# Kernel tuning notes

Measured on AMD Instinct MI355X. Metric: run time of the kernel, lower is better.

Reference implementation:

```python
import jax, jax.numpy as jnp
import numpy as np

B, IMGS, PH, PW = 4, 4, 16, 16      # 4 groups, 4 images/group, 16x16 patches per image
P, C = 16, 3
N = IMGS * PH * PW                   # 1024 packed tokens per group
PATCH_DIM = C * P * P                # 768
DIM, HEADS, DHEAD, DEPTH = 768, 12, 64, 4
INNER = HEADS * DHEAD
MLP = 3072
POSMAX = 32                          # image_size // patch_size
NCLS = 1000
SCALE = DHEAD ** 0.5


def _ln(x, g):
    # torch LayerNorm with learned gamma, beta frozen at 0
    mu = jnp.mean(x, -1, keepdims=True)
    var = jnp.var(x, -1, keepdims=True)
    return (x - mu) * jax.lax.rsqrt(var + 1e-5) * g


def _qk_rmsnorm(t, g):
    # F.normalize(t, dim=-1) * sqrt(dhead) * gamma[h, 1, d]; t: (b,h,n,d), g: (h,d)
    nrm = jnp.sqrt(jnp.sum(t * t, -1, keepdims=True))
    return t / jnp.maximum(nrm, 1e-12) * SCALE * g[None, :, None, :]


def _attention(x, context, ln_g, Wq, Wkv, qg, kg, Wo, attn_mask):
    xn = _ln(x, ln_g)
    kv_in = xn if context is None else context  # context is NOT normed (matches torch)
    q = xn @ Wq
    k, v = jnp.split(kv_in @ Wkv, 2, axis=-1)
    split = lambda t: t.reshape(t.shape[0], t.shape[1], HEADS, DHEAD).transpose(0, 2, 1, 3)
    q, k, v = split(q), split(k), split(v)
    q = _qk_rmsnorm(q, qg)
    k = _qk_rmsnorm(k, kg)
    dots = jnp.einsum('bhid,bhjd->bhij', q, k)  # no 1/sqrt(d): scale lives in RMSNorm
    dots = jnp.where(attn_mask, dots, -jnp.finfo(dots.dtype).max)
    attn = jax.nn.softmax(dots, axis=-1)
    out = jnp.einsum('bhij,bhjd->bhid', attn, v)
    out = out.transpose(0, 2, 1, 3).reshape(x.shape[0], -1, INNER)
    return out @ Wo


def _forward(patches, emb_ln_g, W_emb, b_emb, emb_ln2_g, pos_h, pos_w,
             ln_attn_g, Wq, Wkv, qn_g, kn_g, Wo,
             ln_ff_g, W1, b1, W2, b2, final_ln_g,
             pool_q, pool_ln_g, pWq, pWkv, p_qn_g, p_kn_g, pWo,
             head_ln_g, W_head,
             patch_positions, image_ids, lengths):
    valid = jnp.arange(N)[None, :] < lengths[:, None]              # (B,N) True = real token
    same_img = image_ids[:, :, None] == image_ids[:, None, :]      # (B,i,j) block-diagonal
    attn_mask = (same_img & valid[:, None, :])[:, None]            # (B,1,i,j)

    x = _ln(patches, emb_ln_g) @ W_emb + b_emb
    x = _ln(x, emb_ln2_g)
    x = x + pos_h[patch_positions[..., 0]] + pos_w[patch_positions[..., 1]]

    for l in range(DEPTH):
        x = _attention(x, None, ln_attn_g[l], Wq[l], Wkv[l], qn_g[l], kn_g[l], Wo[l], attn_mask) + x
        h = jax.nn.gelu(_ln(x, ln_ff_g[l]) @ W1[l] + b1[l], approximate=False)
        x = h @ W2[l] + b2[l] + x
    x = _ln(x, final_ln_g)

    # attention pooling: one learned query per packed image
    queries = jnp.broadcast_to(pool_q, (x.shape[0], IMGS, DIM))
    pool_mask = ((jnp.arange(IMGS)[None, :, None] == image_ids[:, None, :]) & valid[:, None, :])[:, None]
    pooled = _attention(queries, x, pool_ln_g, pWq, pWkv, p_qn_g, p_kn_g, pWo, pool_mask) + queries
    return _ln(pooled, head_ln_g) @ W_head  # (B, IMGS, NCLS), mlp_head has no bias


def setup_inputs():
    key = jax.random.key(0)
    ks = jax.random.split(key, 20)
    rn = lambda k, shape, s=0.02: (jax.random.normal(k, shape) * s).astype(jnp.float32)

    patches = jax.random.normal(ks[0], (B, N, PATCH_DIM), dtype=jnp.float32)
    hh, ww = jnp.meshgrid(jnp.arange(PH), jnp.arange(PW), indexing='ij')
    pos = jnp.stack([hh.reshape(-1), ww.reshape(-1)], axis=-1)        # (256,2)
    patch_positions = jnp.broadcast_to(jnp.tile(pos, (IMGS, 1))[None], (B, N, 2)).astype(jnp.int32)
    image_ids = jnp.broadcast_to(jnp.repeat(jnp.arange(IMGS), PH * PW)[None], (B, N)).astype(jnp.int32)
    lengths = jnp.full((B,), N, dtype=jnp.int32)

    return dict(
        patches=patches, patch_positions=patch_positions, image_ids=image_ids, lengths=lengths,
        emb_ln_g=jnp.ones(PATCH_DIM, jnp.float32), W_emb=rn(ks[1], (PATCH_DIM, DIM)),
        b_emb=jnp.zeros(DIM, jnp.float32), emb_ln2_g=jnp.ones(DIM, jnp.float32),
        pos_h=rn(ks[2], (POSMAX, DIM), 1.0), pos_w=rn(ks[3], (POSMAX, DIM), 1.0),
        ln_attn_g=jnp.ones((DEPTH, DIM), jnp.float32),
        Wq=rn(ks[4], (DEPTH, DIM, INNER)), Wkv=rn(ks[5], (DEPTH, DIM, 2 * INNER)),
        qn_g=jnp.ones((DEPTH, HEADS, DHEAD), jnp.float32), kn_g=jnp.ones((DEPTH, HEADS, DHEAD), jnp.float32),
        Wo=rn(ks[6], (DEPTH, INNER, DIM)),
        ln_ff_g=jnp.ones((DEPTH, DIM), jnp.float32),
        W1=rn(ks[7], (DEPTH, DIM, MLP)), b1=jnp.zeros((DEPTH, MLP), jnp.float32),
        W2=rn(ks[8], (DEPTH, MLP, DIM)), b2=jnp.zeros((DEPTH, DIM), jnp.float32),
        final_ln_g=jnp.ones(DIM, jnp.float32),
        pool_q=rn(ks[9], (DIM,), 1.0), pool_ln_g=jnp.ones(DIM, jnp.float32),
        pWq=rn(ks[10], (DIM, INNER)), pWkv=rn(ks[11], (DIM, 2 * INNER)),
        p_qn_g=jnp.ones((HEADS, DHEAD), jnp.float32), p_kn_g=jnp.ones((HEADS, DHEAD), jnp.float32),
        pWo=rn(ks[12], (INNER, DIM)),
        head_ln_g=jnp.ones(DIM, jnp.float32), W_head=rn(ks[13], (DIM, NCLS)),
    )


def reference(patches, patch_positions, image_ids, lengths,
              emb_ln_g, W_emb, b_emb, emb_ln2_g, pos_h, pos_w,
              ln_attn_g, Wq, Wkv, qn_g, kn_g, Wo,
              ln_ff_g, W1, b1, W2, b2, final_ln_g,
              pool_q, pool_ln_g, pWq, pWkv, p_qn_g, p_kn_g, pWo,
              head_ln_g, W_head):
    return _forward(patches, emb_ln_g, W_emb, b_emb, emb_ln2_g, pos_h, pos_w,
                    ln_attn_g, Wq, Wkv, qn_g, kn_g, Wo,
                    ln_ff_g, W1, b1, W2, b2, final_ln_g,
                    pool_q, pool_ln_g, pWq, pWkv, p_qn_g, p_kn_g, pWo,
                    head_ln_g, W_head, patch_positions, image_ids, lengths)
```

## Files before the change

### kernel.cpp

```cpp
#include <hip/hip_runtime.h>
#include <hip/hip_bf16.h>
#include <math.h>

using bf16 = __hip_bfloat16;
typedef short s16x8 __attribute__((ext_vector_type(8)));
typedef float f32x4 __attribute__((ext_vector_type(4)));

#define DEVI __device__ __forceinline__

static constexpr int NB    = 4;
static constexpr int NTOK  = 1024;
static constexpr int DIM   = 768;
static constexpr int NH    = 12;
static constexpr int MLPD  = 3072;
static constexpr int NLAYER= 4;
static constexpr int NIMG  = 4;
static constexpr int NCLS  = 1000;
static constexpr int MR    = NB * NTOK;

DEVI float b2f(bf16 v){ return __bfloat162float(v); }
DEVI bf16  f2b(float v){ return __float2bfloat16(v); }

DEVI void async16(const void* g, void* l) {
  __builtin_amdgcn_global_load_lds((const __attribute__((address_space(1))) void*)g,
                                   (__attribute__((address_space(3))) void*)l, 16, 0, 0);
}

DEVI f32x4 mfma16(s16x8 a, s16x8 b, f32x4 c) {
  return __builtin_amdgcn_mfma_f32_16x16x32_bf16(a, b, c, 0, 0, 0);
}

DEVI float block_sum(float v, float* scratch, int tid) {
  #pragma unroll
  for (int o = 32; o >= 1; o >>= 1) v += __shfl_xor(v, o);
  __syncthreads();
  if ((tid & 63) == 0) scratch[tid >> 6] = v;
  __syncthreads();
  return scratch[0] + scratch[1] + scratch[2] + scratch[3];
}

DEVI float block_max(float v, float* scratch, int tid) {
  #pragma unroll
  for (int o = 32; o >= 1; o >>= 1) v = fmaxf(v, __shfl_xor(v, o));
  __syncthreads();
  if ((tid & 63) == 0) scratch[tid >> 6] = v;
  __syncthreads();
  return fmaxf(fmaxf(scratch[0], scratch[1]), fmaxf(scratch[2], scratch[3]));
}

struct bh4 { bf16 a, b, c, d; };
struct TEntry { const float* src; bf16* dst; int R, C, tiles, tC; };
struct TDesc  { TEntry e[22]; };

__global__ __launch_bounds__(256) void transpose_kernel(TDesc D, int nent) {
  int bid = blockIdx.x, ei = 0;
  while (ei < nent - 1 && bid >= D.e[ei].tiles) { bid -= D.e[ei].tiles; ++ei; }
  const TEntry E = D.e[ei];
  const int tr = bid / E.tC, tc = bid % E.tC;
  __shared__ bf16 t[32][33];
  const int tid = threadIdx.x;
  const int lr = tid >> 3, lc = (tid & 7) * 4;
  const float* srow = E.src + (size_t)(tr*32 + lr)*E.C + tc*32 + lc;
  float4 v = *(const float4*)srow;
  t[lr][lc] = f2b(v.x); t[lr][lc+1] = f2b(v.y); t[lr][lc+2] = f2b(v.z); t[lr][lc+3] = f2b(v.w);
  __syncthreads();
  bh4 o;
  o.a = t[lc+0][lr]; o.b = t[lc+1][lr]; o.c = t[lc+2][lr]; o.d = t[lc+3][lr];
  *(bh4*)(E.dst + (size_t)(tc*32 + lr)*E.R + tr*32 + lc) = o;
}

__global__ __launch_bounds__(256) void ln768_kernel(const float* __restrict__ in,
    const float* __restrict__ g, bf16* __restrict__ out)
{
  __shared__ float scratch[4];
  const int row = blockIdx.x, tid = threadIdx.x;
  const float* p = in + (size_t)row*768;
  const float v0 = p[tid], v1 = p[tid+256], v2 = p[tid+512];
  const float s  = block_sum(v0+v1+v2, scratch, tid);
  const float ss = block_sum(v0*v0+v1*v1+v2*v2, scratch, tid);
  const float mu = s * (1.0f/768.0f);
  const float var = ss * (1.0f/768.0f) - mu*mu;
  const float rstd = rsqrtf(var + 1e-5f);
  bf16* o = out + (size_t)row*768;
  o[tid]     = f2b((v0-mu)*rstd*g[tid]);
  o[tid+256] = f2b((v1-mu)*rstd*g[tid+256]);
  o[tid+512] = f2b((v2-mu)*rstd*g[tid+512]);
}

__global__ __launch_bounds__(256) void ln_pos_kernel(const float* __restrict__ in,
    const float* __restrict__ g, const float* __restrict__ pos_h, const float* __restrict__ pos_w,
    const int* __restrict__ ppos, float* __restrict__ out)
{
  __shared__ float scratch[4];
  const int row = blockIdx.x, tid = threadIdx.x;
  const float* p = in + (size_t)row*768;
  const float v0 = p[tid], v1 = p[tid+256], v2 = p[tid+512];
  const float s  = block_sum(v0+v1+v2, scratch, tid);
  const float ss = block_sum(v0*v0+v1*v1+v2*v2, scratch, tid);
  const float mu = s * (1.0f/768.0f);
  const float rstd = rsqrtf(ss*(1.0f/768.0f) - mu*mu + 1e-5f);
  const int p0 = ppos[row*2], p1 = ppos[row*2+1];
  const float* ph = pos_h + (size_t)p0*768;
  const float* pw = pos_w + (size_t)p1*768;
  float* o = out + (size_t)row*768;
  o[tid]     = (v0-mu)*rstd*g[tid]     + ph[tid]     + pw[tid];
  o[tid+256] = (v1-mu)*rstd*g[tid+256] + ph[tid+256] + pw[tid+256];
  o[tid+512] = (v2-mu)*rstd*g[tid+512] + ph[tid+512] + pw[tid+512];
}

template<int DO_BIAS, int DO_GELU, int OUT_BF16, int DO_RES, int NTILE>
__global__ __launch_bounds__(256)
void gemm_mfma(const bf16* __restrict__ A, const bf16* __restrict__ BT,
               const float* __restrict__ bias, float* __restrict__ Cf,
               bf16* __restrict__ Cb, int M, int Nn, int K)
{
  constexpr int NF = NTILE / 32;
  __shared__ bf16 As[2][64*64];
  __shared__ bf16 Bs[2][(NTILE/2)*64];
  const int tid = threadIdx.x;
  const int wid = tid >> 6, lane = tid & 63;
  const int quad = lane >> 4, l15 = lane & 15;
  const int wy = wid >> 1, wx = wid & 1;
  const int m0 = blockIdx.y * 128, n0 = blockIdx.x * NTILE;
  const int rl = lane >> 3;
  const int cs = lane & 7;

  f32x4 acc[4][NF];
  #pragma unroll
  for (int i = 0; i < 4; ++i)
    #pragma unroll
    for (int j = 0; j < NF; ++j) acc[i][j] = (f32x4){0.f,0.f,0.f,0.f};

  auto stage = [&](int buf, int k0) {
    #pragma unroll
    for (int c = 0; c < 2; ++c) {
      const int rbase = wid*8 + c*32;
      const int r_abs = rbase + rl;
      const int ceff  = cs ^ (r_abs & 7);
      const int mg    = 2*r_abs + (ceff >> 2);
      const int jb    = (ceff & 3) * 16;
      async16((const char*)A + ((size_t)(m0 + mg)*K + k0)*2 + jb, (char*)As[buf] + rbase*128);
    }
    #pragma unroll
    for (int c = 0; c < NTILE/64; ++c) {
      const int rbase = wid*8 + c*32;
      const int r_abs = rbase + rl;
      const int ceff  = cs ^ (r_abs & 7);
      const int ng    = 2*r_abs + (ceff >> 2);
      const int jb    = (ceff & 3) * 16;
      async16((const char*)BT + ((size_t)(n0 + ng)*K + k0)*2 + jb, (char*)Bs[buf] + rbase*128);
    }
  };

  const int nk = K >> 5;
  stage(0, 0);
  for (int kt = 0; kt < nk; ++kt) {
    const int cb = kt & 1;
    __syncthreads();
    if (kt + 1 < nk) stage(cb ^ 1, (kt + 1) << 5);
    s16x8 af[4], bfr[NF];
    #pragma unroll
    for (int mt = 0; mt < 4; ++mt) {
      const int m = wy*64 + mt*16 + l15;
      const int r = m >> 1;
      const int cq = (((m & 1) << 2) | quad) ^ (r & 7);
      af[mt] = *(const s16x8*)((const char*)As[cb] + r*128 + cq*16);
    }
    #pragma unroll
    for (int nt = 0; nt < NF; ++nt) {
      const int n = wx*(NTILE/2) + nt*16 + l15;
      const int r = n >> 1;
      const int cq = (((n & 1) << 2) | quad) ^ (r & 7);
      bfr[nt] = *(const s16x8*)((const char*)Bs[cb] + r*128 + cq*16);
    }
    #pragma unroll
    for (int mt = 0; mt < 4; ++mt)
      #pragma unroll
      for (int nt = 0; nt < NF; ++nt)
        acc[mt][nt] = mfma16(af[mt], bfr[nt], acc[mt][nt]);
  }

  #pragma unroll
  for (int nt = 0; nt < NF; ++nt) {
    const int col = n0 + wx*(NTILE/2) + nt*16 + l15;
    float bv = 0.f;
    if constexpr (DO_BIAS) bv = bias[col];
    #pragma unroll
    for (int mt = 0; mt < 4; ++mt) {
      #pragma unroll
      for (int r = 0; r < 4; ++r) {
        const int row = m0 + wy*64 + mt*16 + quad*4 + r;
        float v = acc[mt][nt][r];
        if constexpr (DO_BIAS) v += bv;
        if constexpr (DO_GELU) v = 0.5f*v*(1.0f + erff(v*0.70710678118654752f));
        const size_t idx = (size_t)row*Nn + col;
        if constexpr (OUT_BF16) Cb[idx] = f2b(v);
        else if constexpr (DO_RES) Cf[idx] += v;
        else Cf[idx] = v;
      }
    }
  }
}

template<int IN_BF16, int DO_BIAS>
__global__ __launch_bounds__(256) void smallm_gemm(const void* __restrict__ Xv,
    const float* __restrict__ W, const float* __restrict__ bias,
    float* __restrict__ out, int Nn)
{
  __shared__ float Xs[16*768];
  __shared__ float red[4][16][64];
  const int tid = threadIdx.x;
  if constexpr (IN_BF16) {
    const bf16* X = (const bf16*)Xv;
    for (int i = tid; i < 16*768; i += 256) Xs[i] = b2f(X[i]);
  } else {
    const float* X = (const float*)Xv;
    for (int i = tid; i < 16*768; i += 256) Xs[i] = X[i];
  }
  __syncthreads();
  const int cl = tid & 63, kg = tid >> 6;
  const int c = blockIdx.x*64 + cl;
  float acc[16];
  #pragma unroll
  for (int r = 0; r < 16; ++r) acc[r] = 0.f;
  if (c < Nn) {
    const int k0 = kg*192;
    #pragma unroll 4
    for (int k = k0; k < k0 + 192; ++k) {
      const float w = W[(size_t)k*Nn + c];
      #pragma unroll
      for (int r = 0; r < 16; ++r) acc[r] += Xs[r*768 + k] * w;
    }
  }
  #pragma unroll
  for (int r = 0; r < 16; ++r) red[kg][r][cl] = acc[r];
  __syncthreads();
  if (kg == 0 && c < Nn) {
    #pragma unroll
    for (int r = 0; r < 16; ++r) {
      float v = red[0][r][cl] + red[1][r][cl] + red[2][r][cl] + red[3][r][cl];
      if constexpr (DO_BIAS) v += bias[c];
      out[(size_t)r*Nn + c] = v;
    }
  }
}

__global__ __launch_bounds__(256) void rms_qkv_kernel(const float* __restrict__ qkv,
    const float* __restrict__ qg, const float* __restrict__ kg,
    bf16* __restrict__ Qb, bf16* __restrict__ Kb, bf16* __restrict__ VTb)
{
  __shared__ float tile[64*68];
  const int nt = blockIdx.x, h = blockIdx.y, b = blockIdx.z;
  const int tid = threadIdx.x;
  const int bh = b*NH + h;
  const size_t rowbase = (size_t)(b*NTOK + nt*64);
  const int r = tid >> 2, pp = tid & 3;

  auto stage = [&](int off) {
    #pragma unroll
    for (int rr = 0; rr < 4; ++rr) {
      const int idx = rr*256 + tid;
      const int rw = idx >> 4, c4 = (idx & 15) << 2;
      float4 val = *(const float4*)(qkv + (rowbase + rw)*2304 + off + c4);
      *(float4*)(&tile[rw*68 + c4]) = val;
    }
  };

  stage(h*64);
  __syncthreads();
  {
    float ssq = 0.f;
    #pragma unroll
    for (int i = 0; i < 16; ++i) { float x = tile[r*68 + pp*16 + i]; ssq += x*x; }
    ssq += __shfl_xor(ssq, 1); ssq += __shfl_xor(ssq, 2);
    const float rn = 8.0f / fmaxf(sqrtf(ssq), 1e-12f);
    bf16* orow = Qb + ((size_t)bh*NTOK + nt*64 + r)*64;
    #pragma unroll
    for (int i = 0; i < 16; ++i) { int d = pp*16+i; orow[d] = f2b(tile[r*68+d]*rn*qg[h*64+d]); }
  }
  __syncthreads();
  stage(768 + h*64);
  __syncthreads();
  {
    float ssq = 0.f;
    #pragma unroll
    for (int i = 0; i < 16; ++i) { float x = tile[r*68 + pp*16 + i]; ssq += x*x; }
    ssq += __shfl_xor(ssq, 1); ssq += __shfl_xor(ssq, 2);
    const float rn = 8.0f / fmaxf(sqrtf(ssq), 1e-12f);
    bf16* orow = Kb + ((size_t)bh*NTOK + nt*64 + r)*64;
    #pragma unroll
    for (int i = 0; i < 16; ++i) { int d = pp*16+i; orow[d] = f2b(tile[r*68+d]*rn*kg[h*64+d]); }
  }
  __syncthreads();
  stage(1536 + h*64);
  __syncthreads();
  {
    const int d = tid >> 2;
    bf16* orow = VTb + ((size_t)bh*64 + d)*NTOK + nt*64;
    #pragma unroll
    for (int i = 0; i < 16; ++i) { int n = pp*16 + i; orow[n] = f2b(tile[n*68 + d]); }
  }
}

__global__ __launch_bounds__(256) void attn_mfma(const bf16* __restrict__ Qb,
    const bf16* __restrict__ Kb, const bf16* __restrict__ VTb, bf16* __restrict__ Ob,
    const int* __restrict__ ids, const int* __restrict__ lens)
{
  __shared__ bf16 Ps[4][16*72];
  __shared__ int  ids_s[NTOK];
  const int qt = blockIdx.x, h = blockIdx.y, b = blockIdx.z;
  const int tid = threadIdx.x;
  const int wid = tid >> 6, lane = tid & 63;
  const int quad = lane >> 4, l15 = lane & 15;
  const int bh = b*NH + h;
  const int q0 = qt*64;
  const int len = lens[b];

  #pragma unroll
  for (int i = 0; i < 4; ++i) ids_s[i*256 + tid] = ids[b*NTOK + i*256 + tid];
  __syncthreads();

  const bf16* qrow = Qb + ((size_t)bh*NTOK + q0 + wid*16 + l15)*64;
  const s16x8 aq0 = *(const s16x8*)(qrow + quad*8);
  const s16x8 aq1 = *(const s16x8*)(qrow + 32 + quad*8);

  int idq[4];
  #pragma unroll
  for (int rr = 0; rr < 4; ++rr) idq[rr] = ids_s[q0 + wid*16 + quad*4 + rr];

  unsigned qm = 0;
  #pragma unroll
  for (int rr = 0; rr < 4; ++rr) qm |= 1u << (idq[rr] & 31);
  #pragma unroll
  for (int o = 32; o >= 1; o >>= 1) qm |= (unsigned)__shfl_xor((int)qm, o);

  f32x4 oacc[4];
  #pragma unroll
  for (int nt = 0; nt < 4; ++nt) oacc[nt] = (f32x4){0.f,0.f,0.f,0.f};
  float mrow[4] = {-3.0e38f,-3.0e38f,-3.0e38f,-3.0e38f};
  float lrow[4] = {0.f,0.f,0.f,0.f};

  const bf16* Kgb = Kb  + (size_t)bh*NTOK*64;
  const bf16* Vgb = VTb + (size_t)bh*64*NTOK;
  bf16* pw = Ps[wid];

  for (int kt = 0; kt < 16; ++kt) {
    const int k0 = kt*64;
    const int idk_l = ids_s[k0 + lane];
    const bool ok = ((k0 + lane) < len) && (((qm >> (idk_l & 31)) & 1u) != 0u);
    if (__ballot(ok) == 0ULL) continue;

    f32x4 sA[4];
    #pragma unroll
    for (int jt = 0; jt < 4; ++jt) {
      const bf16* krow = Kgb + (size_t)(k0 + jt*16 + l15)*64;
      const s16x8 bk0 = *(const s16x8*)(krow + quad*8);
      const s16x8 bk1 = *(const s16x8*)(krow + 32 + quad*8);
      f32x4 s = (f32x4){0.f,0.f,0.f,0.f};
      s = mfma16(aq0, bk0, s);
      s = mfma16(aq1, bk1, s);
      sA[jt] = s;
    }
    #pragma unroll
    for (int jt = 0; jt < 4; ++jt) {
      const int j = k0 + jt*16 + l15;
      const int idk = ids_s[j];
      const bool kvld = j < len;
      #pragma unroll
      for (int rr = 0; rr < 4; ++rr)
        sA[jt][rr] = (kvld && idk == idq[rr]) ? sA[jt][rr] : -3.0e38f;
    }
    float alpha[4], mnew[4];
    #pragma unroll
    for (int rr = 0; rr < 4; ++rr) {
      float mx = fmaxf(fmaxf(sA[0][rr], sA[1][rr]), fmaxf(sA[2][rr], sA[3][rr]));
      mx = fmaxf(mx, __shfl_xor(mx, 1));
      mx = fmaxf(mx, __shfl_xor(mx, 2));
      mx = fmaxf(mx, __shfl_xor(mx, 4));
      mx = fmaxf(mx, __shfl_xor(mx, 8));
      const float mn = fmaxf(mrow[rr], mx);
      mnew[rr] = mn;
      alpha[rr] = expf(mrow[rr] - mn);
      mrow[rr] = mn;
    }
    #pragma unroll
    for (int rr = 0; rr < 4; ++rr) {
      float rs = 0.f;
      #pragma unroll
      for (int jt = 0; jt < 4; ++jt) {
        const float pv = (sA[jt][rr] > -1.0e38f) ? expf(sA[jt][rr] - mnew[rr]) : 0.0f;
        sA[jt][rr] = pv;
        rs += pv;
      }
      rs += __shfl_xor(rs, 1);
      rs += __shfl_xor(rs, 2);
      rs += __shfl_xor(rs, 4);
      rs += __shfl_xor(rs, 8);
      lrow[rr] = lrow[rr]*alpha[rr] + rs;
      #pragma unroll
      for (int nt = 0; nt < 4; ++nt) oacc[nt][rr] *= alpha[rr];
    }
    #pragma unroll
    for (int jt = 0; jt < 4; ++jt)
      #pragma unroll
      for (int rr = 0; rr < 4; ++rr)
        pw[(quad*4+rr)*72 + jt*16 + l15] = f2b(sA[jt][rr]);
    #pragma unroll
    for (int ss = 0; ss < 2; ++ss) {
      const s16x8 ap = *(const s16x8*)(pw + l15*72 + ss*32 + quad*8);
      #pragma unroll
      for (int nt = 0; nt < 4; ++nt) {
        const s16x8 bv = *(const s16x8*)(Vgb + (size_t)(nt*16 + l15)*NTOK + k0 + ss*32 + quad*8);
        oacc[nt] = mfma16(ap, bv, oacc[nt]);
      }
    }
  }

  #pragma unroll
  for (int rr = 0; rr < 4; ++rr) {
    const float inv = lrow[rr] > 0.f ? 1.0f/lrow[rr] : 0.0f;
    const int n = q0 + wid*16 + quad*4 + rr;
    bf16* orow = Ob + ((size_t)b*NTOK + n)*768 + h*64;
    #pragma unroll
    for (int nt = 0; nt < 4; ++nt)
      orow[nt*16 + l15] = f2b(oacc[nt][rr]*inv);
  }
}

__global__ __launch_bounds__(256) void pool_q_kernel(const float* __restrict__ pool_q,
    const float* __restrict__ pool_ln_g, const float* __restrict__ pWq,
    const float* __restrict__ p_qn_g, float* __restrict__ qp)
{
  __shared__ float xn[768];
  __shared__ float scratch[4];
  __shared__ float qraw[64];
  const int h = blockIdx.x, tid = threadIdx.x;
  float v0 = pool_q[tid], v1 = pool_q[tid+256], v2 = pool_q[tid+512];
  const float s  = block_sum(v0+v1+v2, scratch, tid);
  const float ss = block_sum(v0*v0+v1*v1+v2*v2, scratch, tid);
  const float mu = s*(1.0f/768.0f);
  const float rstd = rsqrtf(ss*(1.0f/768.0f) - mu*mu + 1e-5f);
  xn[tid]     = (v0-mu)*rstd*pool_ln_g[tid];
  xn[tid+256] = (v1-mu)*rstd*pool_ln_g[tid+256];
  xn[tid+512] = (v2-mu)*rstd*pool_ln_g[tid+512];
  __syncthreads();
  const int d = tid >> 2, pp = tid & 3;
  const int col = h*64 + d;
  float acc = 0.f;
  for (int k = pp*192; k < (pp+1)*192; ++k) acc += xn[k]*pWq[(size_t)k*768 + col];
  acc += __shfl_xor(acc, 1); acc += __shfl_xor(acc, 2);
  if (pp == 0) qraw[d] = acc;
  __syncthreads();
  if (tid < 64) {
    const float q = qraw[tid];
    float sq = q*q;
    #pragma unroll
    for (int o = 32; o >= 1; o >>= 1) sq += __shfl_xor(sq, o);
    const float rn = 8.0f / fmaxf(sqrtf(sq), 1e-12f);
    qp[h*64 + tid] = q * rn * p_qn_g[h*64 + tid];
  }
}

__global__ __launch_bounds__(256) void pool_attn_kernel(const float* __restrict__ kvp,
    const float* __restrict__ qp, const float* __restrict__ kg,
    const int* __restrict__ ids, const int* __restrict__ lens, float* __restrict__ pooled)
{
  __shared__ float sp[1024];
  __shared__ float qg_s[64];
  __shared__ float scratch[4];
  __shared__ float outred[4][64];
  const int h = blockIdx.x, img = blockIdx.y, b = blockIdx.z;
  const int tid = threadIdx.x;
  const int len = lens[b];
  if (tid < 64) qg_s[tid] = qp[h*64 + tid] * kg[h*64 + tid];
  __syncthreads();

  float smax = -3.0e38f;
  for (int j = tid; j < 1024; j += 256) {
    float sv = -3.0e38f;
    if (j < len && ids[b*NTOK + j] == img) {
      const float* kr = kvp + (size_t)(b*NTOK + j)*1536 + h*64;
      float ssq = 0.f, dq = 0.f;
      #pragma unroll
      for (int dd = 0; dd < 64; dd += 4) {
        float4 k4 = *(const float4*)(kr + dd);
        ssq += k4.x*k4.x + k4.y*k4.y + k4.z*k4.z + k4.w*k4.w;
        dq  += qg_s[dd]*k4.x + qg_s[dd+1]*k4.y + qg_s[dd+2]*k4.z + qg_s[dd+3]*k4.w;
      }
      const float rn = 8.0f / fmaxf(sqrtf(ssq), 1e-12f);
      sv = dq * rn;
    }
    sp[j] = sv;
    smax = fmaxf(smax, sv);
  }
  const float M = block_max(smax, scratch, tid);
  float lsum = 0.f;
  for (int j = tid; j < 1024; j += 256) {
    const float p = (sp[j] > -1.0e38f) ? expf(sp[j] - M) : 0.0f;
    sp[j] = p;
    lsum += p;
  }
  const float L = block_sum(lsum, scratch, tid);
  const float invL = L > 0.f ? 1.0f / L : 0.0f;

  const int d = tid & 63, jg = tid >> 6;
  float acc = 0.f;
  for (int j = jg; j < 1024; j += 4) {
    const float p = sp[j];
    if (p > 0.f) acc += p * kvp[(size_t)(b*NTOK + j)*1536 + 768 + h*64 + d];
  }
  outred[jg][d] = acc;
  __syncthreads();
  if (tid < 64) {
    const float o = (outred[0][tid] + outred[1][tid] + outred[2][tid] + outred[3][tid]) * invL;
    pooled[((size_t)b*NIMG + img)*768 + h*64 + tid] = o;
  }
}

extern "C" void kernel_launch(void* const* d_in, const int* in_sizes, int n_in,
                              void* d_out, int out_size, void* d_ws, size_t ws_size,
                              hipStream_t stream)
{
  const float* patches    = (const float*)d_in[0];
  const int*   ppos       = (const int*)d_in[1];
  const int*   image_ids  = (const int*)d_in[2];
  const int*   lengths    = (const int*)d_in[3];
  const float* emb_ln_g   = (const float*)d_in[4];
  const float* W_emb      = (const float*)d_in[5];
  const float* b_emb      = (const float*)d_in[6];
  const float* emb_ln2_g  = (const float*)d_in[7];
  const float* pos_h      = (const float*)d_in[8];
  const float* pos_w      = (const float*)d_in[9];
  const float* ln_attn_g  = (const float*)d_in[10];
  const float* Wq         = (const float*)d_in[11];
  const float* Wkv        = (const float*)d_in[12];
  const float* qn_g       = (const float*)d_in[13];
  const float* kn_g       = (const float*)d_in[14];
  const float* Wo         = (const float*)d_in[15];
  const float* ln_ff_g    = (const float*)d_in[16];
  const float* W1         = (const float*)d_in[17];
  const float* b1         = (const float*)d_in[18];
  const float* W2         = (const float*)d_in[19];
  const float* b2v        = (const float*)d_in[20];
  const float* final_ln_g = (const float*)d_in[21];
  const float* pool_q     = (const float*)d_in[22];
  const float* pool_ln_g  = (const float*)d_in[23];
  const float* pWq        = (const float*)d_in[24];
  const float* pWkv       = (const float*)d_in[25];
  const float* p_qn_g     = (const float*)d_in[26];
  const float* p_kn_g     = (const float*)d_in[27];
  const float* pWo        = (const float*)d_in[28];
  const float* head_ln_g  = (const float*)d_in[29];
  const float* W_head     = (const float*)d_in[30];

  char* ws = (char*)d_ws;
  size_t off = 0;
  auto alloc = [&](size_t sz){ size_t r = off; off += (sz + 255) & ~(size_t)255; return r; };

  const size_t o_WembT = alloc((size_t)768*768*2);
  size_t o_QKVT[4], o_WoT[4], o_W1T[4], o_W2T[4];
  for (int l = 0; l < NLAYER; ++l) {
    o_QKVT[l] = alloc((size_t)2304*768*2);
    o_WoT[l]  = alloc((size_t)768*768*2);
    o_W1T[l]  = alloc((size_t)3072*768*2);
    o_W2T[l]  = alloc((size_t)768*3072*2);
  }
  const size_t o_pWkvT = alloc((size_t)1536*768*2);
  const size_t o_x     = alloc((size_t)MR*768*4);
  const size_t o_xn    = alloc((size_t)MR*768*2);
  const size_t o_qkv   = alloc((size_t)MR*2304*4);
  const size_t o_Qb    = alloc((size_t)MR*768*2);
  const size_t o_Kb    = alloc((size_t)MR*768*2);
  const size_t o_VT    = alloc((size_t)MR*768*2);
  const size_t o_Ob    = alloc((size_t)MR*768*2);
  const size_t o_qp    = alloc((size_t)768*4);
  const size_t o_pool  = alloc((size_t)16*768*4);
  const size_t o_poolf = alloc((size_t)16*768*4);
  const size_t o_hl    = alloc((size_t)16*768*2);
  if (off > ws_size) return;

  float* x    = (float*)(ws + o_x);
  bf16*  xn   = (bf16*)(ws + o_xn);
  float* qkv  = (float*)(ws + o_qkv);
  bf16*  hb   = (bf16*)(ws + o_qkv);
  bf16*  Qb   = (bf16*)(ws + o_Qb);
  bf16*  Kb   = (bf16*)(ws + o_Kb);
  bf16*  VTb  = (bf16*)(ws + o_VT);
  bf16*  Ob   = (bf16*)(ws + o_Ob);
  float* qp   = (float*)(ws + o_qp);
  float* pooled  = (float*)(ws + o_pool);
  float* pooledf = (float*)(ws + o_poolf);
  bf16*  hl   = (bf16*)(ws + o_hl);

  TDesc td; int ne = 0, total = 0;
  auto add = [&](const float* s, size_t dofs, int R, int C){
    td.e[ne].src = s;
    td.e[ne].dst = (bf16*)(ws + dofs);
    td.e[ne].R = R; td.e[ne].C = C;
    td.e[ne].tiles = (R/32)*(C/32); td.e[ne].tC = C/32;
    total += td.e[ne].tiles; ++ne;
  };
  add(W_emb, o_WembT, 768, 768);
  for (int l = 0; l < NLAYER; ++l) {
    add(Wq  + (size_t)l*768*768,  o_QKVT[l],                 768, 768);
    add(Wkv + (size_t)l*768*1536, o_QKVT[l] + (size_t)768*768*2, 768, 1536);
    add(Wo  + (size_t)l*768*768,  o_WoT[l],                  768, 768);
    add(W1  + (size_t)l*768*3072, o_W1T[l],                  768, 3072);
    add(W2  + (size_t)l*3072*768, o_W2T[l],                  3072, 768);
  }
  add(pWkv, o_pWkvT, 768, 1536);
  transpose_kernel<<<total, 256, 0, stream>>>(td, ne);

  ln768_kernel<<<MR, 256, 0, stream>>>(patches, emb_ln_g, xn);
  gemm_mfma<1,0,0,0,64><<<dim3(12,32), 256, 0, stream>>>(xn, (const bf16*)(ws+o_WembT), b_emb,
                                                         qkv, nullptr, MR, 768, 768);
  ln_pos_kernel<<<MR, 256, 0, stream>>>(qkv, emb_ln2_g, pos_h, pos_w, ppos, x);

  for (int l = 0; l < NLAYER; ++l) {
    ln768_kernel<<<MR, 256, 0, stream>>>(x, ln_attn_g + (size_t)l*768, xn);
    gemm_mfma<0,0,0,0,128><<<dim3(18,32), 256, 0, stream>>>(xn, (const bf16*)(ws+o_QKVT[l]), nullptr,
                                                            qkv, nullptr, MR, 2304, 768);
    rms_qkv_kernel<<<dim3(16,NH,NB), 256, 0, stream>>>(qkv, qn_g + (size_t)l*768, kn_g + (size_t)l*768,
                                                       Qb, Kb, VTb);
    attn_mfma<<<dim3(16,NH,NB), 256, 0, stream>>>(Qb, Kb, VTb, Ob, image_ids, lengths);
    gemm_mfma<0,0,0,1,64><<<dim3(12,32), 256, 0, stream>>>(Ob, (const bf16*)(ws+o_WoT[l]), nullptr,
                                                           x, nullptr, MR, 768, 768);
    ln768_kernel<<<MR, 256, 0, stream>>>(x, ln_ff_g + (size_t)l*768, xn);
    gemm_mfma<1,1,1,0,128><<<dim3(24,32), 256, 0, stream>>>(xn, (const bf16*)(ws+o_W1T[l]), b1 + (size_t)l*3072,
                                                            nullptr, hb, MR, 3072, 768);
    gemm_mfma<1,0,0,1,64><<<dim3(12,32), 256, 0, stream>>>(hb, (const bf16*)(ws+o_W2T[l]), b2v + (size_t)l*768,
                                                           x, nullptr, MR, 768, 3072);
  }

  ln768_kernel<<<MR, 256, 0, stream>>>(x, final_ln_g, xn);
  gemm_mfma<0,0,0,0,128><<<dim3(12,32), 256, 0, stream>>>(xn, (const bf16*)(ws+o_pWkvT), nullptr,
                                                          qkv, nullptr, MR, 1536, 768);
  pool_q_kernel<<<NH, 256, 0, stream>>>(pool_q, pool_ln_g, pWq, p_qn_g, qp);
  pool_attn_kernel<<<dim3(NH,NIMG,NB), 256, 0, stream>>>(qkv, qp, p_kn_g, image_ids, lengths, pooled);
  smallm_gemm<0,1><<<12, 256, 0, stream>>>(pooled, pWo, pool_q, pooledf, 768);
  ln768_kernel<<<16, 256, 0, stream>>>(pooledf, head_ln_g, hl);
  smallm_gemm<1,0><<<16, 256, 0, stream>>>(hl, W_head, nullptr, (float*)d_out, NCLS);
}
```

Measured before the change: 1.176 ms.

## Deepen GEMM LDS pipeline with explicit vmcnt waits and XCD-aware tile swizzle

Replaces the double-buffered GEMM k-loop with a 3- or 4-stage LDS ring. Each step waits with a partial s_waitcnt vmcnt before the barrier, so several tiles of global-to-LDS loads stay in flight while MFMA work runs. It also remaps block IDs so consecutive tiles land on the same XCD, which should improve L2 reuse. The cost is more shared memory, which may lower occupancy. Correctness depends on the hardcoded vmcnt values matching the number of loads per stage.

```diff
diff --git a/kernel.cpp b/kernel.cpp
--- a/kernel.cpp
+++ b/kernel.cpp
@@ -28,6 +28,12 @@
 
 DEVI f32x4 mfma16(s16x8 a, s16x8 b, f32x4 c) {
   return __builtin_amdgcn_mfma_f32_16x16x32_bf16(a, b, c, 0, 0, 0);
+}
+
+template<int N> DEVI void waitcnt_vm() {
+  if constexpr (N == 0)      asm volatile("s_waitcnt vmcnt(0)" ::: "memory");
+  else if constexpr (N == 4) asm volatile("s_waitcnt vmcnt(4)" ::: "memory");
+  else if constexpr (N == 6) asm volatile("s_waitcnt vmcnt(6)" ::: "memory");
 }
 
 DEVI float block_sum(float v, float* scratch, int tid) {
@@ -114,14 +120,24 @@
                const float* __restrict__ bias, float* __restrict__ Cf,
                bf16* __restrict__ Cb, int M, int Nn, int K)
 {
-  constexpr int NF = NTILE / 32;
-  __shared__ bf16 As[2][64*64];
-  __shared__ bf16 Bs[2][(NTILE/2)*64];
+  constexpr int NF  = NTILE / 32;
+  constexpr int PD  = (NTILE == 64) ? 4 : 3;
+  constexpr int VW  = (NTILE == 64) ? 6 : 4;
+  __shared__ bf16 As[PD][64*64];
+  __shared__ bf16 Bs[PD][(NTILE/2)*64];
   const int tid = threadIdx.x;
   const int wid = tid >> 6, lane = tid & 63;
   const int quad = lane >> 4, l15 = lane & 15;
   const int wy = wid >> 1, wx = wid & 1;
-  const int m0 = blockIdx.y * 128, n0 = blockIdx.x * NTILE;
+
+  const int gx  = gridDim.x;
+  const int nwg = gx * gridDim.y;
+  const int bid = blockIdx.y * gx + blockIdx.x;
+  const int qq  = nwg >> 3, rm = nwg & 7;
+  const int xcd = bid & 7,  li = bid >> 3;
+  const int swz = (xcd < rm ? xcd * (qq + 1) : rm * (qq + 1) + (xcd - rm) * qq) + li;
+  const int m0 = (swz / gx) * 128, n0 = (swz % gx) * NTILE;
+
   const int rl = lane >> 3;
   const int cs = lane & 7;
 
@@ -152,12 +168,7 @@
     }
   };
 
-  const int nk = K >> 5;
-  stage(0, 0);
-  for (int kt = 0; kt < nk; ++kt) {
-    const int cb = kt & 1;
-    __syncthreads();
-    if (kt + 1 < nk) stage(cb ^ 1, (kt + 1) << 5);
+  auto compute = [&](int cb) {
     s16x8 af[4], bfr[NF];
     #pragma unroll
     for (int mt = 0; mt < 4; ++mt) {
@@ -178,6 +189,31 @@
       #pragma unroll
       for (int nt = 0; nt < NF; ++nt)
         acc[mt][nt] = mfma16(af[mt], bfr[nt], acc[mt][nt]);
+  };
+
+  const int nk = K >> 5;
+  #pragma unroll
+  for (int t = 0; t < PD - 1; ++t) stage(t, t << 5);
+
+  int cbuf = 0, sbuf = PD - 1;
+  const int mainN = nk - (PD - 1);
+  for (int kt = 0; kt < mainN; ++kt) {
+    __builtin_amdgcn_sched_barrier(0);
+    waitcnt_vm<VW>();
+    __builtin_amdgcn_s_barrier();
+    __builtin_amdgcn_sched_barrier(0);
+    stage(sbuf, (kt + PD - 1) << 5);
+    compute(cbuf);
+    cbuf = (cbuf + 1 == PD) ? 0 : cbuf + 1;
+    sbuf = (sbuf + 1 == PD) ? 0 : sbuf + 1;
+  }
+  for (int kt = mainN; kt < nk; ++kt) {
+    __builtin_amdgcn_sched_barrier(0);
+    waitcnt_vm<0>();
+    __builtin_amdgcn_s_barrier();
+    __builtin_amdgcn_sched_barrier(0);
+    compute(cbuf);
+    cbuf = (cbuf + 1 == PD) ? 0 : cbuf + 1;
   }
 
   #pragma unroll
```

Result: faster. 1.148 ms (-2.4%).
